# Performance work log

Measured on AMD Instinct MI355X. Metric: run time of the kernel, lower is better.

## Reference

```python
import jax, jax.numpy as jnp
import numpy as np

TOPK = 10  # number of start-index candidates probed, as in the torch code


def _reorder_and_flip_edges(edges):
    """Faithful port of reorder_and_flip_edges_torch (start_index=None,
    make_cycle=True, prefer_long_start=True).

    edges: (K, N, D) polylines. Returns (reordered, order, flips, distances).
    """
    K, N, D = edges.shape
    starts = edges[:, 0, :]    # (K, D)
    ends = edges[:, -1, :]     # (K, D)

    # ---- start-index heuristic: probe TOPK longest edges ----
    lengths = jnp.linalg.norm(ends - starts, axis=-1)          # (K,)
    cand = jnp.argsort(-lengths)[: min(TOPK, K)]               # (t,)
    all_pts = jnp.concatenate([starts, ends], axis=0)          # (2K, D)
    cs, ce = starts[cand], ends[cand]                          # (t, D)
    d1 = jnp.linalg.norm(all_pts[None, :, :] - cs[:, None, :], axis=-1).min(axis=1)
    d2 = jnp.linalg.norm(all_pts[None, :, :] - ce[:, None, :], axis=-1).min(axis=1)
    score = jnp.minimum(d1, d2) - 1e-9 * cand.astype(edges.dtype)
    start_index = cand[jnp.argmin(score)]  # strict '<' update in torch == first argmin

    # ---- initial flip: which endpoint is closer to the other edges ----
    s0, e0 = starts[start_index], ends[start_index]
    other = jnp.arange(K) != start_index

    def _min_to_others(pt):
        da = jnp.linalg.norm(pt - starts, axis=1)
        db = jnp.linalg.norm(pt - ends, axis=1)
        return jnp.min(jnp.where(other, jnp.minimum(da, db), jnp.inf))

    use_flip0 = _min_to_others(s0) < _min_to_others(e0)

    used0 = jnp.zeros(K, dtype=bool).at[start_index].set(True)
    cur_end0 = jnp.where(use_flip0, s0, e0)  # end point of the (possibly flipped) first edge

    # ---- sequential greedy nearest-neighbor chaining (K-1 steps) ----
    def step(carry, _):
        used, cur_end = carry
        da = jnp.linalg.norm(cur_end - starts, axis=1)   # dist to each edge's start
        db = jnp.linalg.norm(cur_end - ends, axis=1)     # dist to each edge's end
        md = jnp.where(used, jnp.inf, jnp.minimum(da, db))
        j = jnp.argmin(md)                               # first min == torch tie-break
        flip = da[j] > db[j]                             # connect to end => traverse reversed
        new_end = jnp.where(flip, starts[j], ends[j])
        return (used.at[j].set(True), new_end), (j, flip, md[j])

    (_, _), (js, fl, ds) = jax.lax.scan(step, (used0, cur_end0), None, length=K - 1)

    order = jnp.concatenate([start_index[None], js])     # (K,) int
    flips = jnp.concatenate([use_flip0[None], fl])       # (K,) bool

    gathered = edges[order]                              # (K, N, D)
    reordered = jnp.where(flips[:, None, None], gathered[:, ::-1, :], gathered)

    # make_cycle=True: closing distance last->first
    d_close = jnp.linalg.norm(reordered[-1, -1] - reordered[0, 0])
    distances = jnp.concatenate([ds, d_close[None]])     # (K,)
    return reordered, order, flips, distances


def setup_inputs() -> dict:
    key = jax.random.key(0)
    edges = jax.random.normal(key, (8192, 1024, 3), dtype=jnp.float32)
    return {"edges": edges}


def reference(edges):
    return _reorder_and_flip_edges(edges)
```

## Files before the change

### kernel.cpp

```cpp
#include <hip/hip_runtime.h>
#include <math.h>
#include <float.h>

#define KE 8192
#define NPF 3072
#define NT 512
#define EPT 16
#define NW  8
#define TOPK_N 10
#define KNN 32
#define TAIL_T 7167

typedef unsigned long long u64;
typedef unsigned short u16;
typedef float v2f __attribute__((ext_vector_type(2)));

#define GETP(arr, k) (((k) & 1) ? arr[(k) >> 1].y : arr[(k) >> 1].x)

#define DPPMIN(x, ctrl, rmask)                                              \
  do {                                                                      \
    unsigned _t = (unsigned)__builtin_amdgcn_update_dpp(                    \
        (int)0xFFFFFFFF, (int)(x), (ctrl), (rmask), 0xf, false);            \
    (x) = ((x) < _t) ? (x) : _t;                                            \
  } while (0)

__device__ __forceinline__ float dist2(float ax, float ay, float az,
                                       float bx, float by, float bz) {
#pragma clang fp contract(off)
  float dx = ax - bx, dy = ay - by, dz = az - bz;
  float s = (dx * dx + dy * dy) + dz * dz;
  return s;
}

__device__ __forceinline__ v2f dist2p(v2f cx, v2f cy, v2f cz,
                                      v2f px, v2f py, v2f pz) {
  v2f dx = px - cx, dy = py - cy, dz = pz - cz;
  return __builtin_elementwise_fma(dx, dx,
           __builtin_elementwise_fma(dy, dy, dz * dz));
}

__device__ __forceinline__ float dist2f(float cx, float cy, float cz,
                                        float px, float py, float pz) {
  float dx = px - cx, dy = py - cy, dz = pz - cz;
  return fmaf(dx, dx, fmaf(dy, dy, dz * dz));
}

__device__ __forceinline__ float dist3(float ax, float ay, float az,
                                       float bx, float by, float bz) {
  return sqrtf(dist2(ax, ay, az, bx, by, bz));
}

__device__ __forceinline__ u64 umin64(u64 a, u64 b) { return a < b ? a : b; }

extern "C" __global__ void __launch_bounds__(256)
tbl_build_kernel(const float* __restrict__ edges, float4* __restrict__ tbl4)
{
  int e = blockIdx.x * 256 + threadIdx.x;
  const float* p = edges + (size_t)e * NPF;
  float4 a, b;
  a.x = p[0]; a.y = p[1]; a.z = p[2]; a.w = p[NPF - 3];
  b.x = p[NPF - 2]; b.y = p[NPF - 1]; b.z = 0.f; b.w = 0.f;
  tbl4[(size_t)e * 2]     = a;
  tbl4[(size_t)e * 2 + 1] = b;
}

extern "C" __global__ void __launch_bounds__(64)
knn_kernel(const float4* __restrict__ tbl4, u16* __restrict__ lists)
{
  const int q = blockIdx.x * 64 + threadIdx.x;
  float px, py, pz;
  {
    const float4* tp = tbl4 + (size_t)(q & (KE - 1)) * 2;
    float4 a = tp[0], b = tp[1];
    if (q < KE) { px = a.x; py = a.y; pz = a.z; }
    else        { px = a.w; py = b.x; pz = b.y; }
  }
  const double SENT = __longlong_as_double(0x7FE0000000000000LL);
  double kk[KNN];
#pragma unroll
  for (int i = 0; i < KNN; ++i) kk[i] = SENT;

#pragma unroll 4
  for (int e = 0; e < KE; ++e) {
    float4 a = tbl4[(size_t)e * 2];
    float4 b = tbl4[(size_t)e * 2 + 1];
    float d2s = dist2f(px, py, pz, a.x, a.y, a.z);
    float d2e = dist2f(px, py, pz, a.w, b.x, b.y);
    float v = fminf(d2s, d2e);
    double key = __longlong_as_double(
        (long long)(((u64)__float_as_uint(v) << 32) | (unsigned)e));
    if (key < kk[KNN - 1]) {
      double c = key;
#pragma unroll
      for (int j = 0; j < KNN; ++j) {
        double lo = fmin(kk[j], c);
        c         = fmax(kk[j], c);
        kk[j] = lo;
      }
    }
  }
  u16* lp = lists + (size_t)q * KNN;
#pragma unroll
  for (int i = 0; i < KNN; ++i)
    lp[i] = (u16)((u64)__double_as_longlong(kk[i]) & 0xFFFFu);
}

__device__ void chain_tail(float& cxr, float& cyr, float& czr,
    unsigned* pk_lds, unsigned* d2_lds,
    const float4* s_ta, const float4* s_tb, int lane)
{
  constexpr int E = 16, NPT = 8;
  const int base = lane * E;
  v2f sxp[NPT], syp[NPT], szp[NPT], exp_[NPT], eyp[NPT], ezp[NPT];

#pragma unroll
  for (int e = 0; e < E; ++e) {
    float4 a = s_ta[base + e];
    float4 b = s_tb[base + e];
    if (e & 1) {
      sxp[e >> 1].y = a.x; syp[e >> 1].y = a.y; szp[e >> 1].y = a.z;
      exp_[e >> 1].y = a.w; eyp[e >> 1].y = b.x; ezp[e >> 1].y = b.y;
    } else {
      sxp[e >> 1].x = a.x; syp[e >> 1].x = a.y; szp[e >> 1].x = a.z;
      exp_[e >> 1].x = a.w; eyp[e >> 1].x = b.x; ezp[e >> 1].x = b.y;
    }
  }

  float cx = cxr, cy = cyr, cz = czr;

  for (int t = TAIL_T; t < KE - 1; ++t) {
    v2f cx2 = {cx, cx}, cy2 = {cy, cy}, cz2 = {cz, cz};
    float av0 = INFINITY, av1 = INFINITY, av2 = INFINITY, av3 = INFINITY;
    int   ai0 = 0, ai1 = 0, ai2 = 0, ai3 = 0;
#pragma unroll
    for (int p = 0; p < NPT; ++p) {
      v2f d2s = dist2p(cx2, cy2, cz2, sxp[p], syp[p], szp[p]);
      v2f d2e = dist2p(cx2, cy2, cz2, exp_[p], eyp[p], ezp[p]);
      v2f dm = __builtin_elementwise_min(d2s, d2e);
      int ix = base + 2 * p;
      int iy = base + 2 * p + 1;
      if ((p & 1) == 0) {
        if (dm.x < av0) { av0 = dm.x; ai0 = ix; }
        if (dm.y < av2) { av2 = dm.y; ai2 = iy; }
      } else {
        if (dm.x < av1) { av1 = dm.x; ai1 = ix; }
        if (dm.y < av3) { av3 = dm.y; ai3 = iy; }
      }
    }
    float mv = av0; int mi = ai0;
    if (av1 < mv || (av1 == mv && ai1 < mi)) { mv = av1; mi = ai1; }
    if (av2 < mv || (av2 == mv && ai2 < mi)) { mv = av2; mi = ai2; }
    if (av3 < mv || (av3 == mv && ai3 < mi)) { mv = av3; mi = ai3; }

    unsigned mvb = __float_as_uint(mv);
    unsigned x = mvb;
    DPPMIN(x, 0x111, 0xf);
    DPPMIN(x, 0x112, 0xf);
    DPPMIN(x, 0x114, 0xf);
    DPPMIN(x, 0x118, 0xf);
    DPPMIN(x, 0x142, 0xa);
    DPPMIN(x, 0x143, 0xc);
    unsigned wmin = (unsigned)__builtin_amdgcn_readlane((int)x, 63);

    u64 ball = __ballot(mvb == wmin);
    int win_lane = __ffsll(ball) - 1;
    int wpos = __builtin_amdgcn_readlane(mi, win_lane);

    float4 a = s_ta[wpos];
    float4 b = s_tb[wpos];
    int orig = __float_as_int(b.z);

    float da2 = dist2(cx, cy, cz, a.x, a.y, a.z);
    float db2 = dist2(cx, cy, cz, a.w, b.x, b.y);
    int fl = (sqrtf(da2) > sqrtf(db2)) ? 1 : 0;
    cx = fl ? a.x : a.w;
    cy = fl ? a.y : b.x;
    cz = fl ? a.z : b.y;

    if (lane == win_lane) {
      int e = wpos & (E - 1);
#pragma unroll
      for (int k = 0; k < NPT; ++k) {
        if ((e >> 1) == k) {
          if (e & 1) { sxp[k].y = INFINITY; exp_[k].y = INFINITY; }
          else       { sxp[k].x = INFINITY; exp_[k].x = INFINITY; }
        }
      }
      pk_lds[t + 1] = ((unsigned)orig << 1) | (unsigned)fl;
      d2_lds[t]     = wmin;
    }
  }

  cxr = cx; cyr = cy; czr = cz;
}

extern "C" __global__ void __launch_bounds__(NT, 1)
chain_kernel(const float* __restrict__ edges, float* __restrict__ tail,
             int* __restrict__ ws_order, int* __restrict__ ws_flip,
             float* __restrict__ tbl, const u16* __restrict__ lists)
{
  const int tid = threadIdx.x;
  const int lane = tid & 63;
  const int wid = tid >> 6;
  const int base = tid * EPT;
  const float4* tbl4 = (const float4*)tbl;

  __shared__ __align__(16) u64 kbuf[NW];
  __shared__ float  s_v[NW];
  __shared__ int    s_i[NW];
  __shared__ float  s_m1[NW], s_m2[NW];
  __shared__ unsigned pk_lds[KE];
  __shared__ unsigned d2_lds[KE];
  __shared__ unsigned bm[NW][KE / 32];
  __shared__ __align__(16) float4 s_ta[1024];
  __shared__ __align__(16) float4 s_tb[1024];

  for (int i = lane; i < KE / 32; i += 64) bm[wid][i] = 0u;

  v2f sxp[EPT / 2], syp[EPT / 2], szp[EPT / 2];
  v2f exp_[EPT / 2], eyp[EPT / 2], ezp[EPT / 2];
#pragma unroll
  for (int e = 0; e < EPT; ++e) {
    const float* p = edges + (size_t)(base + e) * NPF;
    float a0 = p[0], a1 = p[1], a2 = p[2];
    float b0 = p[NPF - 3], b1 = p[NPF - 2], b2 = p[NPF - 1];
    if (e & 1) {
      sxp[e >> 1].y = a0; syp[e >> 1].y = a1; szp[e >> 1].y = a2;
      exp_[e >> 1].y = b0; eyp[e >> 1].y = b1; ezp[e >> 1].y = b2;
    } else {
      sxp[e >> 1].x = a0; syp[e >> 1].x = a1; szp[e >> 1].x = a2;
      exp_[e >> 1].x = b0; eyp[e >> 1].x = b1; ezp[e >> 1].x = b2;
    }
  }

  float len[EPT];
#pragma unroll
  for (int e = 0; e < EPT; ++e)
    len[e] = dist3(GETP(exp_, e), GETP(eyp, e), GETP(ezp, e),
                   GETP(sxp, e), GETP(syp, e), GETP(szp, e));

  unsigned tk = 0;
  int start_index = -1;
  for (int r = 0; r < TOPK_N; ++r) {
    float bv = -INFINITY; int bi = 0x7fffffff;
#pragma unroll
    for (int e = 0; e < EPT; ++e) {
      if ((tk >> e) & 1) continue;
      if (len[e] > bv) { bv = len[e]; bi = base + e; }
    }
    for (int m = 1; m < 64; m <<= 1) {
      float v2 = __shfl_xor(bv, m); int i2 = __shfl_xor(bi, m);
      if (v2 > bv || (v2 == bv && i2 < bi)) { bv = v2; bi = i2; }
    }
    if (lane == 0) { s_v[wid] = bv; s_i[wid] = bi; }
    __syncthreads();
    {
      float cv = s_v[lane & (NW - 1)]; int ci = s_i[lane & (NW - 1)];
      for (int m = 1; m < NW; m <<= 1) {
        float v2 = __shfl_xor(cv, m); int i2 = __shfl_xor(ci, m);
        if (v2 > cv || (v2 == cv && i2 < ci)) { cv = v2; ci = i2; }
      }
      int sel = ci;
      if ((sel / EPT) == tid) tk |= 1u << (sel & (EPT - 1));
      if (sel > start_index) start_index = sel;
    }
    __syncthreads();
  }

  float s0x, s0y, s0z, e0x, e0y, e0z;
  {
    const float* p = edges + (size_t)start_index * NPF;
    s0x = p[0];       s0y = p[1];       s0z = p[2];
    e0x = p[NPF - 3]; e0y = p[NPF - 2]; e0z = p[NPF - 1];
  }

  {
    float m1 = INFINITY, m2 = INFINITY;
#pragma unroll
    for (int e = 0; e < EPT; ++e) {
      int k = base + e;
      float a = dist2(s0x, s0y, s0z, GETP(sxp, e), GETP(syp, e), GETP(szp, e));
      float b = dist2(s0x, s0y, s0z, GETP(exp_, e), GETP(eyp, e), GETP(ezp, e));
      float c = dist2(e0x, e0y, e0z, GETP(sxp, e), GETP(syp, e), GETP(szp, e));
      float d = dist2(e0x, e0y, e0z, GETP(exp_, e), GETP(eyp, e), GETP(ezp, e));
      float v1 = fminf(a, b), v2 = fminf(c, d);
      if (k == start_index) { v1 = INFINITY; v2 = INFINITY; }
      m1 = fminf(m1, v1);
      m2 = fminf(m2, v2);
    }
    for (int m = 1; m < 64; m <<= 1) {
      m1 = fminf(m1, __shfl_xor(m1, m));
      m2 = fminf(m2, __shfl_xor(m2, m));
    }
    if (lane == 0) { s_m1[wid] = m1; s_m2[wid] = m2; }
  }
  __syncthreads();

  float cx, cy, cz, fx, fy, fz;
  int flip0;
  {
    float m1 = s_m1[lane & (NW - 1)], m2 = s_m2[lane & (NW - 1)];
    for (int m = 1; m < NW; m <<= 1) {
      m1 = fminf(m1, __shfl_xor(m1, m));
      m2 = fminf(m2, __shfl_xor(m2, m));
    }
    flip0 = (sqrtf(m1) < sqrtf(m2)) ? 1 : 0;
    cx = flip0 ? s0x : e0x;  cy = flip0 ? s0y : e0y;  cz = flip0 ? s0z : e0z;
    fx = flip0 ? e0x : s0x;  fy = flip0 ? e0y : s0y;  fz = flip0 ? e0z : s0z;
    if (tid == 0)
      pk_lds[0] = ((unsigned)start_index << 1) | (unsigned)flip0;
  }
  if (lane == 0)
    bm[wid][start_index >> 5] |= 1u << (start_index & 31);

  if (lists) {
    const float4* lp = (const float4*)lists;
    float acc = 0.f;
    for (int i = tid; i < 65536 + 16384; i += NT) {
      float4 v = (i < 65536) ? lp[i] : tbl4[i - 65536];
      acc += v.x + v.y + v.z + v.w;
    }
    asm volatile("" :: "v"(acc));
  }

  unsigned alive = 0xFFFFu;
  if (tid == (start_index >> 4)) {
    int e = start_index & (EPT - 1);
#pragma unroll
    for (int k = 0; k < EPT / 2; ++k) {
      if ((e >> 1) == k) {
        if (e & 1) { sxp[k].y = INFINITY; exp_[k].y = INFINITY; }
        else       { sxp[k].x = INFINITY; exp_[k].x = INFINITY; }
      }
    }
    alive &= ~(1u << e);
  }
  __syncthreads();

  int pf = 0;
  if (lists) {
    int pid = (lane < 32) ? start_index : start_index + KE;
    pf = (int)lists[(size_t)pid * KNN + (lane & 31)];
  }
  int fl_prev = flip0;

  for (int t = 0; t < TAIL_T; ++t) {
    int widx; unsigned wd2;
    bool hit = false;

    if (lists) {
      int klo = pf;
      float4 ta = tbl4[(size_t)klo * 2];
      float4 tb = tbl4[(size_t)klo * 2 + 1];
      unsigned w = bm[wid][klo >> 5];
      int actwin = fl_prev ? 0 : 1;
      bool unused = ((lane >> 5) == actwin) && !((w >> (klo & 31)) & 1);
      u64 ball = __ballot(unused);
      if (ball) {
        hit = true;
        int first = __ffsll(ball) - 1;
        widx = __builtin_amdgcn_readlane(klo, first);
        float osx = __uint_as_float(__builtin_amdgcn_readlane(__float_as_int(ta.x), first));
        float osy = __uint_as_float(__builtin_amdgcn_readlane(__float_as_int(ta.y), first));
        float osz = __uint_as_float(__builtin_amdgcn_readlane(__float_as_int(ta.z), first));
        float oex = __uint_as_float(__builtin_amdgcn_readlane(__float_as_int(ta.w), first));
        float oey = __uint_as_float(__builtin_amdgcn_readlane(__float_as_int(tb.x), first));
        float oez = __uint_as_float(__builtin_amdgcn_readlane(__float_as_int(tb.y), first));
        if (lane == 0)
          bm[wid][widx >> 5] |= 1u << (widx & 31);
        float d2s = dist2f(cx, cy, cz, osx, osy, osz);
        float d2e = dist2f(cx, cy, cz, oex, oey, oez);
        wd2 = __float_as_uint(fminf(d2s, d2e));
        float da2 = dist2(cx, cy, cz, osx, osy, osz);
        float db2 = dist2(cx, cy, cz, oex, oey, oez);
        int fl = (sqrtf(da2) > sqrtf(db2)) ? 1 : 0;
        cx = fl ? osx : oex;
        cy = fl ? osy : oey;
        cz = fl ? osz : oez;
        int pid = (lane < 32) ? widx : widx + KE;
        pf = (int)lists[(size_t)pid * KNN + (lane & 31)];
        if (wid == 0 && lane == 0) {
          pk_lds[t + 1] = ((unsigned)widx << 1) | (unsigned)fl;
          d2_lds[t] = wd2;
        }
        if (tid == (widx >> 4)) {
          int e = widx & (EPT - 1);
#pragma unroll
          for (int k = 0; k < EPT / 2; ++k) {
            if ((e >> 1) == k) {
              if (e & 1) { sxp[k].y = INFINITY; exp_[k].y = INFINITY; }
              else       { sxp[k].x = INFINITY; exp_[k].x = INFINITY; }
            }
          }
          alive &= ~(1u << e);
        }
        fl_prev = fl;
      }
    }

    if (!hit) {
      v2f cx2 = {cx, cx}, cy2 = {cy, cy}, cz2 = {cz, cz};
      float av0 = INFINITY, av1 = INFINITY, av2 = INFINITY, av3 = INFINITY;
      int   ai0 = 0, ai1 = 0, ai2 = 0, ai3 = 0;
#pragma unroll
      for (int p = 0; p < EPT / 2; ++p) {
        v2f d2s = dist2p(cx2, cy2, cz2, sxp[p], syp[p], szp[p]);
        v2f d2e = dist2p(cx2, cy2, cz2, exp_[p], eyp[p], ezp[p]);
        v2f dm = __builtin_elementwise_min(d2s, d2e);
        int ix = base + 2 * p;
        int iy = base + 2 * p + 1;
        if ((p & 1) == 0) {
          if (dm.x < av0) { av0 = dm.x; ai0 = ix; }
          if (dm.y < av2) { av2 = dm.y; ai2 = iy; }
        } else {
          if (dm.x < av1) { av1 = dm.x; ai1 = ix; }
          if (dm.y < av3) { av3 = dm.y; ai3 = iy; }
        }
      }
      float mv = av0; int mi = ai0;
      if (av1 < mv || (av1 == mv && ai1 < mi)) { mv = av1; mi = ai1; }
      if (av2 < mv || (av2 == mv && ai2 < mi)) { mv = av2; mi = ai2; }
      if (av3 < mv || (av3 == mv && ai3 < mi)) { mv = av3; mi = ai3; }

      unsigned mvb = __float_as_uint(mv);
      unsigned x = mvb;
      DPPMIN(x, 0x111, 0xf);
      DPPMIN(x, 0x112, 0xf);
      DPPMIN(x, 0x114, 0xf);
      DPPMIN(x, 0x118, 0xf);
      DPPMIN(x, 0x142, 0xa);
      DPPMIN(x, 0x143, 0xc);
      unsigned wmin = (unsigned)__builtin_amdgcn_readlane((int)x, 63);
      u64 ball2 = __ballot(mvb == wmin);
      int win_lane = __ffsll(ball2) - 1;
      if (lane == win_lane)
        kbuf[wid] = ((u64)wmin << 32) | (unsigned)mi;
      __syncthreads();
      const ulonglong2* kp = (const ulonglong2*)&kbuf[0];
      ulonglong2 q0 = kp[0], q1 = kp[1], q2 = kp[2], q3 = kp[3];
      u64 kb = umin64(umin64(umin64(q0.x, q0.y), umin64(q1.x, q1.y)),
                      umin64(umin64(q2.x, q2.y), umin64(q3.x, q3.y)));
      widx = __builtin_amdgcn_readfirstlane((int)(kb & 0xFFFFFFFFu));
      wd2 = (unsigned)(kb >> 32);
      __syncthreads();

      float osx, osy, osz, oex, oey, oez;
      if (tbl4) {
        float4 a = tbl4[(size_t)widx * 2], b = tbl4[(size_t)widx * 2 + 1];
        osx = a.x; osy = a.y; osz = a.z; oex = a.w; oey = b.x; oez = b.y;
      } else {
        const float* wp = edges + (size_t)widx * NPF;
        osx = wp[0]; osy = wp[1]; osz = wp[2];
        oex = wp[NPF - 3]; oey = wp[NPF - 2]; oez = wp[NPF - 1];
      }
      float da2 = dist2(cx, cy, cz, osx, osy, osz);
      float db2 = dist2(cx, cy, cz, oex, oey, oez);
      int fl = (sqrtf(da2) > sqrtf(db2)) ? 1 : 0;
      cx = fl ? osx : oex;
      cy = fl ? osy : oey;
      cz = fl ? osz : oez;

      if (lane == 0) {
        bm[wid][widx >> 5] |= 1u << (widx & 31);
        if (wid == 0) {
          pk_lds[t + 1] = ((unsigned)widx << 1) | (unsigned)fl;
          d2_lds[t] = wd2;
        }
      }
      if (tid == (widx >> 4)) {
        int e = widx & (EPT - 1);
#pragma unroll
        for (int k = 0; k < EPT / 2; ++k) {
          if ((e >> 1) == k) {
            if (e & 1) { sxp[k].y = INFINITY; exp_[k].y = INFINITY; }
            else       { sxp[k].x = INFINITY; exp_[k].x = INFINITY; }
          }
        }
        alive &= ~(1u << e);
      }
      if (lists) {
        int pid = (lane < 32) ? widx : widx + KE;
        pf = (int)lists[(size_t)pid * KNN + (lane & 31)];
      }
      fl_prev = fl;
    }
  }

  __syncthreads();
  {
    int cnt = __popc(alive);
    int sc = cnt;
#pragma unroll
    for (int m = 1; m < 64; m <<= 1) {
      int o = __shfl_up(sc, m);
      if (lane >= m) sc += o;
    }
    if (lane == 63) s_i[wid] = sc;
    __syncthreads();
    int wbase = 0;
#pragma unroll
    for (int w = 0; w < NW; ++w)
      if (w < wid) wbase += s_i[w];
    int pos = wbase + sc - cnt;
#pragma unroll
    for (int e = 0; e < EPT; ++e) {
      if ((alive >> e) & 1) {
        float4 a, b;
        a.x = GETP(sxp, e); a.y = GETP(syp, e); a.z = GETP(szp, e);
        a.w = GETP(exp_, e);
        b.x = GETP(eyp, e); b.y = GETP(ezp, e);
        b.z = __int_as_float(base + e); b.w = 0.f;
        s_ta[pos] = a; s_tb[pos] = b; ++pos;
      }
    }
  }
  __syncthreads();

  if (wid == 0) {
    chain_tail(cx, cy, cz, pk_lds, d2_lds, s_ta, s_tb, lane);
    if (lane == 0)
      d2_lds[KE - 1] = __float_as_uint(dist2(cx, cy, cz, fx, fy, fz));
  }
  __syncthreads();

  float* ord_f = tail;
  float* flp_f = tail + KE;
  float* dst_f = tail + 2 * KE;
#pragma unroll
  for (int k = 0; k < EPT; ++k) {
    int i = tid + k * NT;
    unsigned p = pk_lds[i];
    int w = (int)(p >> 1);
    int f = (int)(p & 1u);
    ord_f[i] = (float)w;
    flp_f[i] = (float)f;
    dst_f[i] = sqrtf(__uint_as_float(d2_lds[i]));
    ws_order[i] = w;
    ws_flip[i]  = f;
  }
}

extern "C" __global__ void __launch_bounds__(256)
gather_kernel(const float* __restrict__ edges, const int* __restrict__ ws_order,
              const int* __restrict__ ws_flip, float* __restrict__ out)
{
  int idx = blockIdx.x * 256 + threadIdx.x;
  int i = idx / NPF;
  int f = idx - i * NPF;
  int o  = ws_order[i];
  int fl = ws_flip[i];
  int r = f / 3;
  int c = f - r * 3;
  int srcf = fl ? ((1023 - r) * 3 + c) : f;
  out[idx] = edges[o * NPF + srcf];
}

extern "C" void kernel_launch(void* const* d_in, const int* in_sizes, int n_in,
                              void* d_out, int out_size, void* d_ws, size_t ws_size,
                              hipStream_t stream) {
  (void)in_sizes; (void)n_in; (void)out_size;
  const float* edges = (const float*)d_in[0];
  float* out  = (float*)d_out;
  float* tail = out + (size_t)KE * NPF;
  int* ws_order = (int*)d_ws;
  int* ws_flip  = ws_order + KE;

  size_t off_tbl = (size_t)2 * KE * sizeof(int);
  size_t off_lst = off_tbl + (size_t)KE * 8 * sizeof(float);
  size_t need_lst = off_lst + (size_t)2 * KE * KNN * sizeof(u16);

  float* tbl   = (ws_size >= off_lst) ? (float*)((char*)d_ws + off_tbl) : nullptr;
  u16*   lists = (ws_size >= need_lst && tbl) ? (u16*)((char*)d_ws + off_lst)
                                              : nullptr;

  if (tbl)
    hipLaunchKernelGGL(tbl_build_kernel, dim3(KE / 256), dim3(256), 0, stream,
                       edges, (float4*)tbl);
  if (lists)
    hipLaunchKernelGGL(knn_kernel, dim3(2 * KE / 64), dim3(64), 0, stream,
                       (const float4*)tbl, lists);
  hipLaunchKernelGGL(chain_kernel, dim3(1), dim3(NT), 0, stream,
                     edges, tail, ws_order, ws_flip, tbl, (const u16*)lists);
  hipLaunchKernelGGL(gather_kernel, dim3((KE * NPF) / 256), dim3(256), 0, stream,
                     edges, ws_order, ws_flip, out);
}
```

Before: 5.918 ms.

## Double KNN candidate list to 64 to raise fast-path hit rate in chaining

Each point's precomputed nearest-neighbour list grows from 32 to 64 entries, and the serial chain loop checks both halves with two ballots, loading the endpoint table only when the match comes from the second half. The goal is more greedy steps resolved from the candidate list, so fewer steps fall back to the full block-wide argmin over all edges. In exchange the KNN kernel keeps twice as many candidates per thread (more registers and work), its block size changes from 64 to 256 threads, and each chain step does extra global loads. The cache warm-up loop is also widened to cover the larger list.

```diff
diff --git a/kernel.cpp b/kernel.cpp
--- a/kernel.cpp
+++ b/kernel.cpp
@@ -8,7 +8,7 @@
 #define EPT 16
 #define NW  8
 #define TOPK_N 10
-#define KNN 32
+#define KNN 64
 #define TAIL_T 7167
 
 typedef unsigned long long u64;
@@ -23,6 +23,8 @@
         (int)0xFFFFFFFF, (int)(x), (ctrl), (rmask), 0xf, false);            \
     (x) = ((x) < _t) ? (x) : _t;                                            \
   } while (0)
+
+#define RDL(v, l) __uint_as_float((unsigned)__builtin_amdgcn_readlane(__float_as_int(v), (l)))
 
 __device__ __forceinline__ float dist2(float ax, float ay, float az,
                                        float bx, float by, float bz) {
@@ -64,10 +66,10 @@
   tbl4[(size_t)e * 2 + 1] = b;
 }
 
-extern "C" __global__ void __launch_bounds__(64)
+extern "C" __global__ void __launch_bounds__(256)
 knn_kernel(const float4* __restrict__ tbl4, u16* __restrict__ lists)
 {
-  const int q = blockIdx.x * 64 + threadIdx.x;
+  const int q = blockIdx.x * 256 + threadIdx.x;
   float px, py, pz;
   {
     const float4* tp = tbl4 + (size_t)(q & (KE - 1)) * 2;
@@ -316,8 +318,8 @@
   if (lists) {
     const float4* lp = (const float4*)lists;
     float acc = 0.f;
-    for (int i = tid; i < 65536 + 16384; i += NT) {
-      float4 v = (i < 65536) ? lp[i] : tbl4[i - 65536];
+    for (int i = tid; i < 131072 + 16384; i += NT) {
+      float4 v = (i < 131072) ? lp[i] : tbl4[i - 131072];
       acc += v.x + v.y + v.z + v.w;
     }
     asm volatile("" :: "v"(acc));
@@ -337,10 +339,11 @@
   }
   __syncthreads();
 
-  int pf = 0;
+  int pf0 = 0, pf1 = 0;
   if (lists) {
     int pid = (lane < 32) ? start_index : start_index + KE;
-    pf = (int)lists[(size_t)pid * KNN + (lane & 31)];
+    pf0 = (int)lists[(size_t)pid * KNN + (lane & 31)];
+    pf1 = (int)lists[(size_t)pid * KNN + 32 + (lane & 31)];
   }
   int fl_prev = flip0;
 
@@ -349,23 +352,31 @@
     bool hit = false;
 
     if (lists) {
-      int klo = pf;
-      float4 ta = tbl4[(size_t)klo * 2];
-      float4 tb = tbl4[(size_t)klo * 2 + 1];
-      unsigned w = bm[wid][klo >> 5];
+      int klo0 = pf0, klo1 = pf1;
+      float4 ta = tbl4[(size_t)klo0 * 2];
+      float4 tb = tbl4[(size_t)klo0 * 2 + 1];
+      unsigned w0 = bm[wid][klo0 >> 5];
+      unsigned w1 = bm[wid][klo1 >> 5];
       int actwin = fl_prev ? 0 : 1;
-      bool unused = ((lane >> 5) == actwin) && !((w >> (klo & 31)) & 1);
-      u64 ball = __ballot(unused);
-      if (ball) {
+      bool act = ((lane >> 5) == actwin);
+      bool un0 = act && !((w0 >> (klo0 & 31)) & 1);
+      bool un1 = act && !((w1 >> (klo1 & 31)) & 1);
+      u64 b0 = __ballot(un0);
+      u64 b1 = __ballot(un1);
+      if (b0 | b1) {
         hit = true;
-        int first = __ffsll(ball) - 1;
-        widx = __builtin_amdgcn_readlane(klo, first);
-        float osx = __uint_as_float(__builtin_amdgcn_readlane(__float_as_int(ta.x), first));
-        float osy = __uint_as_float(__builtin_amdgcn_readlane(__float_as_int(ta.y), first));
-        float osz = __uint_as_float(__builtin_amdgcn_readlane(__float_as_int(ta.z), first));
-        float oex = __uint_as_float(__builtin_amdgcn_readlane(__float_as_int(ta.w), first));
-        float oey = __uint_as_float(__builtin_amdgcn_readlane(__float_as_int(tb.x), first));
-        float oez = __uint_as_float(__builtin_amdgcn_readlane(__float_as_int(tb.y), first));
+        float osx, osy, osz, oex, oey, oez;
+        if (b0) {
+          int first = __ffsll(b0) - 1;
+          widx = __builtin_amdgcn_readlane(klo0, first);
+          osx = RDL(ta.x, first); osy = RDL(ta.y, first); osz = RDL(ta.z, first);
+          oex = RDL(ta.w, first); oey = RDL(tb.x, first); oez = RDL(tb.y, first);
+        } else {
+          int first = __ffsll(b1) - 1;
+          widx = __builtin_amdgcn_readlane(klo1, first);
+          float4 a = tbl4[(size_t)widx * 2], b_ = tbl4[(size_t)widx * 2 + 1];
+          osx = a.x; osy = a.y; osz = a.z; oex = a.w; oey = b_.x; oez = b_.y;
+        }
         if (lane == 0)
           bm[wid][widx >> 5] |= 1u << (widx & 31);
         float d2s = dist2f(cx, cy, cz, osx, osy, osz);
@@ -378,7 +389,8 @@
         cy = fl ? osy : oey;
         cz = fl ? osz : oez;
         int pid = (lane < 32) ? widx : widx + KE;
-        pf = (int)lists[(size_t)pid * KNN + (lane & 31)];
+        pf0 = (int)lists[(size_t)pid * KNN + (lane & 31)];
+        pf1 = (int)lists[(size_t)pid * KNN + 32 + (lane & 31)];
         if (wid == 0 && lane == 0) {
           pk_lds[t + 1] = ((unsigned)widx << 1) | (unsigned)fl;
           d2_lds[t] = wd2;
@@ -480,7 +492,8 @@
       }
       if (lists) {
         int pid = (lane < 32) ? widx : widx + KE;
-        pf = (int)lists[(size_t)pid * KNN + (lane & 31)];
+        pf0 = (int)lists[(size_t)pid * KNN + (lane & 31)];
+        pf1 = (int)lists[(size_t)pid * KNN + 32 + (lane & 31)];
       }
       fl_prev = fl;
     }
@@ -577,7 +590,7 @@
     hipLaunchKernelGGL(tbl_build_kernel, dim3(KE / 256), dim3(256), 0, stream,
                        edges, (float4*)tbl);
   if (lists)
-    hipLaunchKernelGGL(knn_kernel, dim3(2 * KE / 64), dim3(64), 0, stream,
+    hipLaunchKernelGGL(knn_kernel, dim3(2 * KE / 256), dim3(256), 0, stream,
                        (const float4*)tbl, lists);
   hipLaunchKernelGGL(chain_kernel, dim3(1), dim3(NT), 0, stream,
                      edges, tail, ws_order, ws_flip, tbl, (const u16*)lists);
```

Measured after the change: 7.736 ms, median of 2. 1.31x slower.

## Split KNN candidate search into partitioned partial lists plus merge kernel

Applied to the files above, without the earlier changes.

The per-endpoint 32-nearest-edge search is split into four partitions of the edge set, each computed by a separate block group, then merged in a second kernel. The old version ran 256 blocks of 64 threads, each scanning all 8192 edges. The new one runs 256 blocks of 256 threads, each scanning 2048 edges, which exposes more parallelism and shortens each thread's serial scan. The cost is an extra launch, a large u64 workspace for the partial lists, and a merge pass. The path is used only when the workspace is big enough.

```diff
diff --git a/kernel.cpp b/kernel.cpp
--- a/kernel.cpp
+++ b/kernel.cpp
@@ -9,6 +9,7 @@
 #define NW  8
 #define TOPK_N 10
 #define KNN 32
+#define NPART 4
 #define TAIL_T 7167
 
 typedef unsigned long long u64;
@@ -23,6 +24,8 @@
         (int)0xFFFFFFFF, (int)(x), (ctrl), (rmask), 0xf, false);            \
     (x) = ((x) < _t) ? (x) : _t;                                            \
   } while (0)
+
+#define RDL(v, l) __uint_as_float((unsigned)__builtin_amdgcn_readlane(__float_as_int(v), (l)))
 
 __device__ __forceinline__ float dist2(float ax, float ay, float az,
                                        float bx, float by, float bz) {
@@ -103,6 +106,72 @@
 #pragma unroll
   for (int i = 0; i < KNN; ++i)
     lp[i] = (u16)((u64)__double_as_longlong(kk[i]) & 0xFFFFu);
+}
+
+extern "C" __global__ void __launch_bounds__(256)
+knn_partial_kernel(const float4* __restrict__ tbl4, u64* __restrict__ plists)
+{
+  const int part = blockIdx.x >> 6;
+  const int q = (blockIdx.x & 63) * 256 + threadIdx.x;
+  const int e0 = part * (KE / NPART);
+  float px, py, pz;
+  {
+    const float4* tp = tbl4 + (size_t)(q & (KE - 1)) * 2;
+    float4 a = tp[0], b = tp[1];
+    if (q < KE) { px = a.x; py = a.y; pz = a.z; }
+    else        { px = a.w; py = b.x; pz = b.y; }
+  }
+  const double SENT = __longlong_as_double(0x7FE0000000000000LL);
+  double kk[KNN];
+#pragma unroll
+  for (int i = 0; i < KNN; ++i) kk[i] = SENT;
+
+#pragma unroll 4
+  for (int ee = 0; ee < KE / NPART; ++ee) {
+    int e = e0 + ee;
+    float4 a = tbl4[(size_t)e * 2];
+    float4 b = tbl4[(size_t)e * 2 + 1];
+    float d2s = dist2f(px, py, pz, a.x, a.y, a.z);
+    float d2e = dist2f(px, py, pz, a.w, b.x, b.y);
+    float v = fminf(d2s, d2e);
+    double key = __longlong_as_double(
+        (long long)(((u64)__float_as_uint(v) << 32) | (unsigned)e));
+    if (key < kk[KNN - 1]) {
+      double c = key;
+#pragma unroll
+      for (int j = 0; j < KNN; ++j) {
+        double lo = fmin(kk[j], c);
+        c         = fmax(kk[j], c);
+        kk[j] = lo;
+      }
+    }
+  }
+  u64* lp = plists + ((size_t)q * NPART + part) * KNN;
+#pragma unroll
+  for (int i = 0; i < KNN; ++i)
+    lp[i] = (u64)__double_as_longlong(kk[i]);
+}
+
+extern "C" __global__ void __launch_bounds__(256)
+knn_merge_kernel(const u64* __restrict__ plists, u16* __restrict__ lists)
+{
+  const int q = blockIdx.x * 256 + threadIdx.x;
+  const u64* p0 = plists + ((size_t)q * NPART + 0) * KNN;
+  const u64* p1 = plists + ((size_t)q * NPART + 1) * KNN;
+  const u64* p2 = plists + ((size_t)q * NPART + 2) * KNN;
+  const u64* p3 = plists + ((size_t)q * NPART + 3) * KNN;
+  u64 h0 = p0[0], h1 = p1[0], h2 = p2[0], h3 = p3[0];
+  int i0 = 1, i1 = 1, i2 = 1, i3 = 1;
+  u16* lp = lists + (size_t)q * KNN;
+#pragma unroll 1
+  for (int j = 0; j < KNN; ++j) {
+    u64 m = umin64(umin64(h0, h1), umin64(h2, h3));
+    lp[j] = (u16)(m & 0xFFFFu);
+    if (m == h0)      h0 = (i0 < KNN) ? p0[i0++] : ~0ull;
+    else if (m == h1) h1 = (i1 < KNN) ? p1[i1++] : ~0ull;
+    else if (m == h2) h2 = (i2 < KNN) ? p2[i2++] : ~0ull;
+    else              h3 = (i3 < KNN) ? p3[i3++] : ~0ull;
+  }
 }
 
 __device__ void chain_tail(float& cxr, float& cyr, float& czr,
@@ -360,12 +429,8 @@
         hit = true;
         int first = __ffsll(ball) - 1;
         widx = __builtin_amdgcn_readlane(klo, first);
-        float osx = __uint_as_float(__builtin_amdgcn_readlane(__float_as_int(ta.x), first));
-        float osy = __uint_as_float(__builtin_amdgcn_readlane(__float_as_int(ta.y), first));
-        float osz = __uint_as_float(__builtin_amdgcn_readlane(__float_as_int(ta.z), first));
-        float oex = __uint_as_float(__builtin_amdgcn_readlane(__float_as_int(ta.w), first));
-        float oey = __uint_as_float(__builtin_amdgcn_readlane(__float_as_int(tb.x), first));
-        float oez = __uint_as_float(__builtin_amdgcn_readlane(__float_as_int(tb.y), first));
+        float osx = RDL(ta.x, first), osy = RDL(ta.y, first), osz = RDL(ta.z, first);
+        float oex = RDL(ta.w, first), oey = RDL(tb.x, first), oez = RDL(tb.y, first);
         if (lane == 0)
           bm[wid][widx >> 5] |= 1u << (widx & 31);
         float d2s = dist2f(cx, cy, cz, osx, osy, osz);
@@ -565,20 +630,30 @@
   int* ws_order = (int*)d_ws;
   int* ws_flip  = ws_order + KE;
 
-  size_t off_tbl = (size_t)2 * KE * sizeof(int);
-  size_t off_lst = off_tbl + (size_t)KE * 8 * sizeof(float);
-  size_t need_lst = off_lst + (size_t)2 * KE * KNN * sizeof(u16);
+  size_t off_tbl  = (size_t)2 * KE * sizeof(int);
+  size_t off_lst  = off_tbl + (size_t)KE * 8 * sizeof(float);
+  size_t off_part = off_lst + (size_t)2 * KE * KNN * sizeof(u16);
+  size_t need_lst  = off_part;
+  size_t need_part = off_part + (size_t)2 * KE * NPART * KNN * sizeof(u64);
 
   float* tbl   = (ws_size >= off_lst) ? (float*)((char*)d_ws + off_tbl) : nullptr;
   u16*   lists = (ws_size >= need_lst && tbl) ? (u16*)((char*)d_ws + off_lst)
                                               : nullptr;
+  u64*   plists = (ws_size >= need_part && lists)
+                    ? (u64*)((char*)d_ws + off_part) : nullptr;
 
   if (tbl)
     hipLaunchKernelGGL(tbl_build_kernel, dim3(KE / 256), dim3(256), 0, stream,
                        edges, (float4*)tbl);
-  if (lists)
+  if (plists) {
+    hipLaunchKernelGGL(knn_partial_kernel, dim3(64 * NPART), dim3(256), 0,
+                       stream, (const float4*)tbl, plists);
+    hipLaunchKernelGGL(knn_merge_kernel, dim3(2 * KE / 256), dim3(256), 0,
+                       stream, (const u64*)plists, lists);
+  } else if (lists) {
     hipLaunchKernelGGL(knn_kernel, dim3(2 * KE / 64), dim3(64), 0, stream,
                        (const float4*)tbl, lists);
+  }
   hipLaunchKernelGGL(chain_kernel, dim3(1), dim3(NT), 0, stream,
                      edges, tail, ws_order, ws_flip, tbl, (const u16*)lists);
   hipLaunchKernelGGL(gather_kernel, dim3((KE * NPF) / 256), dim3(256), 0, stream,
```

Result: faster. 4.978 ms (-15.9%).
